# Performance work log

Measured on AMD Instinct MI355X. Metric: run time of the kernel, lower is better.

Reference implementation:

```python
import jax, jax.numpy as jnp
import numpy as np

N, E, G = 50000, 800000, 100
H, C = 4, 64


def _gatv2(x, src, dst, ea, Wl, bl, Wr, br, We, att, bias):
    # PyG GATv2Conv: x_l = lin_l(x) (source side), x_r = lin_r(x) (target side)
    xl = (x @ Wl + bl).reshape(-1, H, C)
    xr = (x @ Wr + br).reshape(-1, H, C)
    e = (ea @ We).reshape(-1, H, C)               # [E,H,C]
    m = jax.nn.leaky_relu(xl[src] + xr[dst] + e, negative_slope=0.2)
    alpha = jnp.einsum('ehc,hc->eh', m, att)      # [E,H]
    amax = jax.ops.segment_max(alpha, dst, num_segments=N)
    amax = jnp.where(jnp.isfinite(amax), amax, jnp.float32(0.0))
    ex = jnp.exp(alpha - amax[dst])
    denom = jax.ops.segment_sum(ex, dst, num_segments=N)
    a = ex / (denom[dst] + jnp.float32(1e-16))    # segment softmax over in-edges
    out = jax.ops.segment_sum(xl[src] * a[..., None], dst, num_segments=N)
    return out.reshape(N, H * C) + bias


def setup_inputs() -> dict:
    key = jax.random.key(0)
    ks = jax.random.split(key, 24)
    lin = lambda k, i, o: (jax.random.normal(k, (i, o), jnp.float32) / np.sqrt(i).astype(np.float32))
    x = jax.random.normal(ks[0], (N, 8), jnp.float32)
    edge_index = jnp.stack([jax.random.randint(ks[1], (E,), 0, N),
                            jax.random.randint(ks[2], (E,), 0, N)])
    edge_attr = jax.random.normal(ks[3], (E, 1), jnp.float32)
    batch = jnp.sort(jax.random.randint(ks[4], (N,), 0, G))
    return dict(
        x=x, edge_index=edge_index, edge_attr=edge_attr, batch=batch,
        enc_W=lin(ks[5], 8, 64), enc_b=jnp.zeros((64,), jnp.float32),
        g1_Wl=lin(ks[6], 64, 256), g1_bl=jnp.zeros((256,), jnp.float32),
        g1_Wr=lin(ks[7], 64, 256), g1_br=jnp.zeros((256,), jnp.float32),
        g1_We=lin(ks[8], 1, 256),
        g1_att=jax.random.normal(ks[9], (H, C), jnp.float32) / np.sqrt(C).astype(np.float32),
        g1_bias=jnp.zeros((256,), jnp.float32),
        g2_Wl=lin(ks[10], 256, 256), g2_bl=jnp.zeros((256,), jnp.float32),
        g2_Wr=lin(ks[11], 256, 256), g2_br=jnp.zeros((256,), jnp.float32),
        g2_We=lin(ks[12], 1, 256),
        g2_att=jax.random.normal(ks[13], (H, C), jnp.float32) / np.sqrt(C).astype(np.float32),
        g2_bias=jnp.zeros((256,), jnp.float32),
        p1_W=lin(ks[14], 256, 128), p1_b=jnp.zeros((128,), jnp.float32),
        ln_g=jnp.ones((128,), jnp.float32), ln_b=jnp.zeros((128,), jnp.float32),
        p2_W=lin(ks[15], 128, 64), p2_b=jnp.zeros((64,), jnp.float32),
    )


def reference(x, edge_index, edge_attr, batch,
              enc_W, enc_b,
              g1_Wl, g1_bl, g1_Wr, g1_br, g1_We, g1_att, g1_bias,
              g2_Wl, g2_bl, g2_Wr, g2_br, g2_We, g2_att, g2_bias,
              p1_W, p1_b, ln_g, ln_b, p2_W, p2_b):
    src, dst = edge_index[0], edge_index[1]
    h = jax.nn.relu(x @ enc_W + enc_b)
    h = jax.nn.relu(_gatv2(h, src, dst, edge_attr, g1_Wl, g1_bl, g1_Wr, g1_br, g1_We, g1_att, g1_bias))
    h = jax.nn.relu(_gatv2(h, src, dst, edge_attr, g2_Wl, g2_bl, g2_Wr, g2_br, g2_We, g2_att, g2_bias))
    # global mean pool over graphs
    sums = jax.ops.segment_sum(h, batch, num_segments=G)
    cnt = jax.ops.segment_sum(jnp.ones((N, 1), h.dtype), batch, num_segments=G)
    p = sums / jnp.maximum(cnt, jnp.float32(1.0))
    # post MLP (dropout is identity in eval)
    z = p @ p1_W + p1_b
    mu = jnp.mean(z, axis=-1, keepdims=True)
    var = jnp.mean(jnp.square(z - mu), axis=-1, keepdims=True)
    z = (z - mu) * jax.lax.rsqrt(var + jnp.float32(1e-5)) * ln_g + ln_b
    z = jax.nn.relu(z)
    return jax.nn.relu(z @ p2_W + p2_b)
```

## Files before the change

### kernel.cpp

```cpp
#include <hip/hip_runtime.h>

#define NH 4
#define CH 64

__global__ void encoder_kernel(const float* __restrict__ x, const float* __restrict__ W,
                               const float* __restrict__ b, float* __restrict__ h, int N) {
  int idx = blockIdx.x * blockDim.x + threadIdx.x;
  if (idx >= N * 64) return;
  int n = idx >> 6, j = idx & 63;
  const float* xp = x + n * 8;
  float acc = b[j];
#pragma unroll
  for (int k = 0; k < 8; ++k) acc = fmaf(xp[k], W[k * 64 + j], acc);
  h[idx] = fmaxf(acc, 0.0f);
}

template <int K>
__global__ void lin_lr_kernel(const float* __restrict__ h,
                              const float* __restrict__ Wl, const float* __restrict__ bl,
                              const float* __restrict__ Wr, const float* __restrict__ br,
                              float* __restrict__ xl, float* __restrict__ xr, int N) {
  __shared__ float hs[8][K];
  int n0 = blockIdx.x * 8;
  int j = threadIdx.x;
  int nmax = N - n0; if (nmax > 8) nmax = 8;
  for (int idx = j; idx < nmax * K; idx += 256) {
    int m = idx / K, k = idx % K;
    hs[m][k] = h[(size_t)(n0 + m) * K + k];
  }
  __syncthreads();
  float accl[8], accr[8];
  float bjl = bl[j], bjr = br[j];
#pragma unroll
  for (int m = 0; m < 8; ++m) { accl[m] = bjl; accr[m] = bjr; }
  for (int k = 0; k < K; ++k) {
    float wl = Wl[k * 256 + j];
    float wr = Wr[k * 256 + j];
#pragma unroll
    for (int m = 0; m < 8; ++m) {
      accl[m] = fmaf(hs[m][k], wl, accl[m]);
      accr[m] = fmaf(hs[m][k], wr, accr[m]);
    }
  }
  for (int m = 0; m < nmax; ++m) {
    xl[(size_t)(n0 + m) * 256 + j] = accl[m];
    xr[(size_t)(n0 + m) * 256 + j] = accr[m];
  }
}

__global__ void hist_kernel(const int* __restrict__ dst, int* __restrict__ deg, int E) {
  int e = blockIdx.x * blockDim.x + threadIdx.x;
  if (e < E) atomicAdd(&deg[dst[e]], 1);
}

__global__ void scan_partial_kernel(const int* __restrict__ deg, int* __restrict__ partial, int N) {
  __shared__ int sm[256];
  int t = threadIdx.x;
  int i = blockIdx.x * 256 + t;
  sm[t] = (i < N) ? deg[i] : 0;
  __syncthreads();
#pragma unroll
  for (int s = 128; s > 0; s >>= 1) {
    if (t < s) sm[t] += sm[t + s];
    __syncthreads();
  }
  if (t == 0) partial[blockIdx.x] = sm[0];
}

__global__ void scan_offsets_kernel(int* __restrict__ partial, int nb) {
  __shared__ int sm[256];
  int t = threadIdx.x;
  int v = (t < nb) ? partial[t] : 0;
  sm[t] = v;
  __syncthreads();
#pragma unroll
  for (int off = 1; off < 256; off <<= 1) {
    int a = (t >= off) ? sm[t - off] : 0;
    __syncthreads();
    sm[t] += a;
    __syncthreads();
  }
  if (t < nb) partial[t] = sm[t] - v;
}

__global__ void scan_final_kernel(const int* __restrict__ deg, const int* __restrict__ partial,
                                  int* __restrict__ rowptr, int* __restrict__ cursor, int N, int E) {
  __shared__ int sm[256];
  int t = threadIdx.x;
  int i = blockIdx.x * 256 + t;
  int v = (i < N) ? deg[i] : 0;
  sm[t] = v;
  __syncthreads();
#pragma unroll
  for (int off = 1; off < 256; off <<= 1) {
    int a = (t >= off) ? sm[t - off] : 0;
    __syncthreads();
    sm[t] += a;
    __syncthreads();
  }
  if (i < N) {
    int ex = partial[blockIdx.x] + sm[t] - v;
    rowptr[i] = ex;
    cursor[i] = ex;
  }
  if (i == 0) rowptr[N] = E;
}

__global__ void scatter_build_kernel(const int* __restrict__ src, const int* __restrict__ dst,
                                     const float* __restrict__ ea, int* __restrict__ cursor,
                                     int* __restrict__ srcs, float* __restrict__ eas, int E) {
  int e = blockIdx.x * blockDim.x + threadIdx.x;
  if (e >= E) return;
  int d = dst[e];
  int pos = atomicAdd(&cursor[d], 1);
  srcs[pos] = src[e];
  eas[pos] = ea[e];
}

__device__ __forceinline__ void edge_accum(const float4 xlv, const float eav,
                                           const float4 xr4, const float4 We4, const float4 at4,
                                           float4& acc, float& denom) {
  float4 v;
  v.x = fmaf(eav, We4.x, xlv.x + xr4.x);
  v.y = fmaf(eav, We4.y, xlv.y + xr4.y);
  v.z = fmaf(eav, We4.z, xlv.z + xr4.z);
  v.w = fmaf(eav, We4.w, xlv.w + xr4.w);
  v.x = (v.x >= 0.f) ? v.x : 0.2f * v.x;
  v.y = (v.y >= 0.f) ? v.y : 0.2f * v.y;
  v.z = (v.z >= 0.f) ? v.z : 0.2f * v.z;
  v.w = (v.w >= 0.f) ? v.w : 0.2f * v.w;
  float p = v.x * at4.x + v.y * at4.y + v.z * at4.z + v.w * at4.w;
  p += __shfl_xor(p, 1, 64);
  p += __shfl_xor(p, 2, 64);
  p += __shfl_xor(p, 4, 64);
  p += __shfl_xor(p, 8, 64);
  float ex = __expf(p);
  denom += ex;
  acc.x = fmaf(ex, xlv.x, acc.x);
  acc.y = fmaf(ex, xlv.y, acc.y);
  acc.z = fmaf(ex, xlv.z, acc.z);
  acc.w = fmaf(ex, xlv.w, acc.w);
}

template <bool POOL>
__global__ void gat_aggregate_kernel(const int* __restrict__ rowptr,
                                     const int* __restrict__ srcs,
                                     const float* __restrict__ eas,
                                     const float* __restrict__ xl,
                                     const float* __restrict__ xr,
                                     const float* __restrict__ We,
                                     const float* __restrict__ att,
                                     const float* __restrict__ bias,
                                     float* __restrict__ out,
                                     const int* __restrict__ batch,
                                     float* __restrict__ sums,
                                     float* __restrict__ cnt,
                                     int N) {
  int d = (int)((blockIdx.x * (size_t)blockDim.x + threadIdx.x) >> 6);
  int lane = threadIdx.x & 63;
  if (d >= N) return;
  const float4* xl4p = (const float4*)xl;
  float4 xr4 = ((const float4*)xr)[(size_t)d * 64 + lane];
  float4 We4 = ((const float4*)We)[lane];
  float4 at4 = ((const float4*)att)[lane];
  int beg = rowptr[d], end = rowptr[d + 1];
  float4 acc = {0.f, 0.f, 0.f, 0.f};
  float denom = 0.f;
  int i = beg;
  for (; i + 3 < end; i += 4) {
    int s0 = srcs[i], s1 = srcs[i + 1], s2 = srcs[i + 2], s3 = srcs[i + 3];
    float e0 = eas[i], e1 = eas[i + 1], e2 = eas[i + 2], e3 = eas[i + 3];
    float4 a0 = xl4p[(size_t)s0 * 64 + lane];
    float4 a1 = xl4p[(size_t)s1 * 64 + lane];
    float4 a2 = xl4p[(size_t)s2 * 64 + lane];
    float4 a3 = xl4p[(size_t)s3 * 64 + lane];
    edge_accum(a0, e0, xr4, We4, at4, acc, denom);
    edge_accum(a1, e1, xr4, We4, at4, acc, denom);
    edge_accum(a2, e2, xr4, We4, at4, acc, denom);
    edge_accum(a3, e3, xr4, We4, at4, acc, denom);
  }
  for (; i < end; ++i) {
    int s0 = srcs[i];
    float e0 = eas[i];
    float4 a0 = xl4p[(size_t)s0 * 64 + lane];
    edge_accum(a0, e0, xr4, We4, at4, acc, denom);
  }
  float inv = 1.f / (denom + 1e-16f);
  float4 b4 = ((const float4*)bias)[lane];
  float4 o;
  o.x = fmaxf(fmaf(acc.x, inv, b4.x), 0.f);
  o.y = fmaxf(fmaf(acc.y, inv, b4.y), 0.f);
  o.z = fmaxf(fmaf(acc.z, inv, b4.z), 0.f);
  o.w = fmaxf(fmaf(acc.w, inv, b4.w), 0.f);
  if (POOL) {
    int g = batch[d];
    float* sg = sums + (size_t)g * 256 + lane * 4;
    atomicAdd(sg + 0, o.x);
    atomicAdd(sg + 1, o.y);
    atomicAdd(sg + 2, o.z);
    atomicAdd(sg + 3, o.w);
    if (lane == 0) atomicAdd(&cnt[g], 1.0f);
  } else {
    ((float4*)out)[(size_t)d * 64 + lane] = o;
  }
}

__global__ void mlp_kernel(const float* __restrict__ sums, const float* __restrict__ cnt,
                           const float* __restrict__ p1W, const float* __restrict__ p1b,
                           const float* __restrict__ lng, const float* __restrict__ lnb,
                           const float* __restrict__ p2W, const float* __restrict__ p2b,
                           float* __restrict__ outp, int G) {
  __shared__ float p[256];
  __shared__ float z[128];
  __shared__ float wsum[2];
  __shared__ float wsum2[2];
  int g = blockIdx.x;
  int t = threadIdx.x;
  float c = fmaxf(cnt[g], 1.0f);
  p[t] = sums[(size_t)g * 256 + t] / c;
  p[t + 128] = sums[(size_t)g * 256 + t + 128] / c;
  __syncthreads();
  float acc = p1b[t];
  for (int k = 0; k < 256; ++k) acc = fmaf(p[k], p1W[k * 128 + t], acc);
  float v = acc;
#pragma unroll
  for (int off = 32; off > 0; off >>= 1) v += __shfl_xor(v, off, 64);
  if ((t & 63) == 0) wsum[t >> 6] = v;
  __syncthreads();
  float mu = (wsum[0] + wsum[1]) * (1.0f / 128.0f);
  float dv = acc - mu;
  float vv = dv * dv;
#pragma unroll
  for (int off = 32; off > 0; off >>= 1) vv += __shfl_xor(vv, off, 64);
  if ((t & 63) == 0) wsum2[t >> 6] = vv;
  __syncthreads();
  float var = (wsum2[0] + wsum2[1]) * (1.0f / 128.0f);
  float zv = dv * rsqrtf(var + 1e-5f) * lng[t] + lnb[t];
  z[t] = fmaxf(zv, 0.0f);
  __syncthreads();
  if (t < 64) {
    float o = p2b[t];
    for (int k = 0; k < 128; ++k) o = fmaf(z[k], p2W[k * 64 + t], o);
    outp[(size_t)g * 64 + t] = fmaxf(o, 0.0f);
  }
}

extern "C" void kernel_launch(void* const* d_in, const int* in_sizes, int n_in,
                              void* d_out, int out_size, void* d_ws, size_t ws_size,
                              hipStream_t stream) {
  const float* x      = (const float*)d_in[0];
  const int*   ei     = (const int*)d_in[1];
  const float* ea     = (const float*)d_in[2];
  const int*   batch  = (const int*)d_in[3];
  const float* enc_W  = (const float*)d_in[4];
  const float* enc_b  = (const float*)d_in[5];
  const float* Wl1    = (const float*)d_in[6];
  const float* bl1    = (const float*)d_in[7];
  const float* Wr1    = (const float*)d_in[8];
  const float* br1    = (const float*)d_in[9];
  const float* We1    = (const float*)d_in[10];
  const float* att1   = (const float*)d_in[11];
  const float* bias1  = (const float*)d_in[12];
  const float* Wl2    = (const float*)d_in[13];
  const float* bl2    = (const float*)d_in[14];
  const float* Wr2    = (const float*)d_in[15];
  const float* br2    = (const float*)d_in[16];
  const float* We2    = (const float*)d_in[17];
  const float* att2   = (const float*)d_in[18];
  const float* bias2  = (const float*)d_in[19];
  const float* p1W    = (const float*)d_in[20];
  const float* p1b    = (const float*)d_in[21];
  const float* lng    = (const float*)d_in[22];
  const float* lnb    = (const float*)d_in[23];
  const float* p2W    = (const float*)d_in[24];
  const float* p2b    = (const float*)d_in[25];
  float* outp = (float*)d_out;

  int N = in_sizes[0] / 8;
  int E = in_sizes[2];
  int G = out_size / 64;
  const int* src = ei;
  const int* dst = ei + E;
  int nb = (N + 255) / 256;

  float* ws      = (float*)d_ws;
  float* h0      = ws;
  float* B0      = h0     + (size_t)N * 64;
  float* B1      = B0     + (size_t)N * 256;
  float* B2      = B1     + (size_t)N * 256;
  float* eas     = B2     + (size_t)N * 256;
  float* sums    = eas    + (size_t)E;
  float* cnt     = sums   + (size_t)G * 256;
  int*   srcs    = (int*)(cnt + G);
  int*   rowptr  = srcs + (size_t)E;
  int*   cursor  = rowptr + (size_t)(N + 1);
  int*   partial = cursor + (size_t)N;

  encoder_kernel<<<(N * 64 + 255) / 256, 256, 0, stream>>>(x, enc_W, enc_b, h0, N);

  hipMemsetAsync(cursor, 0, (size_t)N * sizeof(int), stream);
  hist_kernel<<<(E + 255) / 256, 256, 0, stream>>>(dst, cursor, E);
  scan_partial_kernel<<<nb, 256, 0, stream>>>(cursor, partial, N);
  scan_offsets_kernel<<<1, 256, 0, stream>>>(partial, nb);
  scan_final_kernel<<<nb, 256, 0, stream>>>(cursor, partial, rowptr, cursor, N, E);
  scatter_build_kernel<<<(E + 255) / 256, 256, 0, stream>>>(src, dst, ea, cursor, srcs, eas, E);

  lin_lr_kernel<64><<<(N + 7) / 8, 256, 0, stream>>>(h0, Wl1, bl1, Wr1, br1, B0, B1, N);
  gat_aggregate_kernel<false><<<(N + 3) / 4, 256, 0, stream>>>(
      rowptr, srcs, eas, B0, B1, We1, att1, bias1, B2, nullptr, nullptr, nullptr, N);

  lin_lr_kernel<256><<<(N + 7) / 8, 256, 0, stream>>>(B2, Wl2, bl2, Wr2, br2, B0, B1, N);
  hipMemsetAsync(sums, 0, ((size_t)G * 256 + G) * sizeof(float), stream);
  gat_aggregate_kernel<true><<<(N + 3) / 4, 256, 0, stream>>>(
      rowptr, srcs, eas, B0, B1, We2, att2, bias2, nullptr, batch, sums, cnt, N);

  mlp_kernel<<<G, 128, 0, stream>>>(sums, cnt, p1W, p1b, lng, lnb, p2W, p2b, outp, G);
}
```

Before: 1.036 ms.

## Store source features in bf16 and pack edge src/attr into int2

The source-side projection xl is written as bf16 and widened back to float inside the aggregation, which halves the bytes of the random gather that dominates the edge loop. Edge source index and attribute are packed into a single int2 array so each edge costs one load instead of two. The main loop is unrolled to 8 edges, with a 2-edge and a 1-edge tail, to keep more gathers in flight. The cost is bf16 rounding error on xl, which feeds both the attention logits and the aggregated messages.

```diff
diff --git a/kernel.cpp b/kernel.cpp
--- a/kernel.cpp
+++ b/kernel.cpp
@@ -2,6 +2,14 @@
 
 #define NH 4
 #define CH 64
+
+__device__ __forceinline__ float bf2f(unsigned short u) {
+  return __uint_as_float(((unsigned)u) << 16);
+}
+__device__ __forceinline__ unsigned short f2bf(float f) {
+  unsigned b = __float_as_uint(f);
+  return (unsigned short)((b + 0x7fffu + ((b >> 16) & 1u)) >> 16);
+}
 
 __global__ void encoder_kernel(const float* __restrict__ x, const float* __restrict__ W,
                                const float* __restrict__ b, float* __restrict__ h, int N) {
@@ -19,7 +27,7 @@
 __global__ void lin_lr_kernel(const float* __restrict__ h,
                               const float* __restrict__ Wl, const float* __restrict__ bl,
                               const float* __restrict__ Wr, const float* __restrict__ br,
-                              float* __restrict__ xl, float* __restrict__ xr, int N) {
+                              unsigned short* __restrict__ xlb, float* __restrict__ xr, int N) {
   __shared__ float hs[8][K];
   int n0 = blockIdx.x * 8;
   int j = threadIdx.x;
@@ -43,7 +51,7 @@
     }
   }
   for (int m = 0; m < nmax; ++m) {
-    xl[(size_t)(n0 + m) * 256 + j] = accl[m];
+    xlb[(size_t)(n0 + m) * 256 + j] = f2bf(accl[m]);
     xr[(size_t)(n0 + m) * 256 + j] = accr[m];
   }
 }
@@ -108,18 +116,19 @@
 
 __global__ void scatter_build_kernel(const int* __restrict__ src, const int* __restrict__ dst,
                                      const float* __restrict__ ea, int* __restrict__ cursor,
-                                     int* __restrict__ srcs, float* __restrict__ eas, int E) {
+                                     int2* __restrict__ edg, int E) {
   int e = blockIdx.x * blockDim.x + threadIdx.x;
   if (e >= E) return;
   int d = dst[e];
   int pos = atomicAdd(&cursor[d], 1);
-  srcs[pos] = src[e];
-  eas[pos] = ea[e];
-}
-
-__device__ __forceinline__ void edge_accum(const float4 xlv, const float eav,
+  edg[pos] = make_int2(src[e], __float_as_int(ea[e]));
+}
+
+__device__ __forceinline__ void edge_accum(const ushort4 xu, const float eav,
                                            const float4 xr4, const float4 We4, const float4 at4,
                                            float4& acc, float& denom) {
+  float4 xlv;
+  xlv.x = bf2f(xu.x); xlv.y = bf2f(xu.y); xlv.z = bf2f(xu.z); xlv.w = bf2f(xu.w);
   float4 v;
   v.x = fmaf(eav, We4.x, xlv.x + xr4.x);
   v.y = fmaf(eav, We4.y, xlv.y + xr4.y);
@@ -144,9 +153,8 @@
 
 template <bool POOL>
 __global__ void gat_aggregate_kernel(const int* __restrict__ rowptr,
-                                     const int* __restrict__ srcs,
-                                     const float* __restrict__ eas,
-                                     const float* __restrict__ xl,
+                                     const int2* __restrict__ edg,
+                                     const unsigned short* __restrict__ xlb,
                                      const float* __restrict__ xr,
                                      const float* __restrict__ We,
                                      const float* __restrict__ att,
@@ -159,7 +167,7 @@
   int d = (int)((blockIdx.x * (size_t)blockDim.x + threadIdx.x) >> 6);
   int lane = threadIdx.x & 63;
   if (d >= N) return;
-  const float4* xl4p = (const float4*)xl;
+  const ushort4* xlp = (const ushort4*)xlb;
   float4 xr4 = ((const float4*)xr)[(size_t)d * 64 + lane];
   float4 We4 = ((const float4*)We)[lane];
   float4 at4 = ((const float4*)att)[lane];
@@ -167,23 +175,37 @@
   float4 acc = {0.f, 0.f, 0.f, 0.f};
   float denom = 0.f;
   int i = beg;
-  for (; i + 3 < end; i += 4) {
-    int s0 = srcs[i], s1 = srcs[i + 1], s2 = srcs[i + 2], s3 = srcs[i + 3];
-    float e0 = eas[i], e1 = eas[i + 1], e2 = eas[i + 2], e3 = eas[i + 3];
-    float4 a0 = xl4p[(size_t)s0 * 64 + lane];
-    float4 a1 = xl4p[(size_t)s1 * 64 + lane];
-    float4 a2 = xl4p[(size_t)s2 * 64 + lane];
-    float4 a3 = xl4p[(size_t)s3 * 64 + lane];
-    edge_accum(a0, e0, xr4, We4, at4, acc, denom);
-    edge_accum(a1, e1, xr4, We4, at4, acc, denom);
-    edge_accum(a2, e2, xr4, We4, at4, acc, denom);
-    edge_accum(a3, e3, xr4, We4, at4, acc, denom);
-  }
-  for (; i < end; ++i) {
-    int s0 = srcs[i];
-    float e0 = eas[i];
-    float4 a0 = xl4p[(size_t)s0 * 64 + lane];
-    edge_accum(a0, e0, xr4, We4, at4, acc, denom);
+  for (; i + 7 < end; i += 8) {
+    int2 e0 = edg[i], e1 = edg[i + 1], e2 = edg[i + 2], e3 = edg[i + 3];
+    int2 e4 = edg[i + 4], e5 = edg[i + 5], e6 = edg[i + 6], e7 = edg[i + 7];
+    ushort4 a0 = xlp[(size_t)e0.x * 64 + lane];
+    ushort4 a1 = xlp[(size_t)e1.x * 64 + lane];
+    ushort4 a2 = xlp[(size_t)e2.x * 64 + lane];
+    ushort4 a3 = xlp[(size_t)e3.x * 64 + lane];
+    ushort4 a4 = xlp[(size_t)e4.x * 64 + lane];
+    ushort4 a5 = xlp[(size_t)e5.x * 64 + lane];
+    ushort4 a6 = xlp[(size_t)e6.x * 64 + lane];
+    ushort4 a7 = xlp[(size_t)e7.x * 64 + lane];
+    edge_accum(a0, __int_as_float(e0.y), xr4, We4, at4, acc, denom);
+    edge_accum(a1, __int_as_float(e1.y), xr4, We4, at4, acc, denom);
+    edge_accum(a2, __int_as_float(e2.y), xr4, We4, at4, acc, denom);
+    edge_accum(a3, __int_as_float(e3.y), xr4, We4, at4, acc, denom);
+    edge_accum(a4, __int_as_float(e4.y), xr4, We4, at4, acc, denom);
+    edge_accum(a5, __int_as_float(e5.y), xr4, We4, at4, acc, denom);
+    edge_accum(a6, __int_as_float(e6.y), xr4, We4, at4, acc, denom);
+    edge_accum(a7, __int_as_float(e7.y), xr4, We4, at4, acc, denom);
+  }
+  for (; i + 1 < end; i += 2) {
+    int2 e0 = edg[i], e1 = edg[i + 1];
+    ushort4 a0 = xlp[(size_t)e0.x * 64 + lane];
+    ushort4 a1 = xlp[(size_t)e1.x * 64 + lane];
+    edge_accum(a0, __int_as_float(e0.y), xr4, We4, at4, acc, denom);
+    edge_accum(a1, __int_as_float(e1.y), xr4, We4, at4, acc, denom);
+  }
+  if (i < end) {
+    int2 e0 = edg[i];
+    ushort4 a0 = xlp[(size_t)e0.x * 64 + lane];
+    edge_accum(a0, __int_as_float(e0.y), xr4, We4, at4, acc, denom);
   }
   float inv = 1.f / (denom + 1e-16f);
   float4 b4 = ((const float4*)bias)[lane];
@@ -285,14 +307,13 @@
 
   float* ws      = (float*)d_ws;
   float* h0      = ws;
-  float* B0      = h0     + (size_t)N * 64;
-  float* B1      = B0     + (size_t)N * 256;
+  float* B1      = h0     + (size_t)N * 64;
   float* B2      = B1     + (size_t)N * 256;
-  float* eas     = B2     + (size_t)N * 256;
-  float* sums    = eas    + (size_t)E;
+  float* sums    = B2     + (size_t)N * 256;
   float* cnt     = sums   + (size_t)G * 256;
-  int*   srcs    = (int*)(cnt + G);
-  int*   rowptr  = srcs + (size_t)E;
+  unsigned short* xlb = (unsigned short*)(cnt + G);
+  int2*  edg     = (int2*)(xlb + (size_t)N * 256);
+  int*   rowptr  = (int*)(edg + (size_t)E);
   int*   cursor  = rowptr + (size_t)(N + 1);
   int*   partial = cursor + (size_t)N;
 
@@ -303,16 +324,16 @@
   scan_partial_kernel<<<nb, 256, 0, stream>>>(cursor, partial, N);
   scan_offsets_kernel<<<1, 256, 0, stream>>>(partial, nb);
   scan_final_kernel<<<nb, 256, 0, stream>>>(cursor, partial, rowptr, cursor, N, E);
-  scatter_build_kernel<<<(E + 255) / 256, 256, 0, stream>>>(src, dst, ea, cursor, srcs, eas, E);
-
-  lin_lr_kernel<64><<<(N + 7) / 8, 256, 0, stream>>>(h0, Wl1, bl1, Wr1, br1, B0, B1, N);
+  scatter_build_kernel<<<(E + 255) / 256, 256, 0, stream>>>(src, dst, ea, cursor, edg, E);
+
+  lin_lr_kernel<64><<<(N + 7) / 8, 256, 0, stream>>>(h0, Wl1, bl1, Wr1, br1, xlb, B1, N);
   gat_aggregate_kernel<false><<<(N + 3) / 4, 256, 0, stream>>>(
-      rowptr, srcs, eas, B0, B1, We1, att1, bias1, B2, nullptr, nullptr, nullptr, N);
-
-  lin_lr_kernel<256><<<(N + 7) / 8, 256, 0, stream>>>(B2, Wl2, bl2, Wr2, br2, B0, B1, N);
+      rowptr, edg, xlb, B1, We1, att1, bias1, B2, nullptr, nullptr, nullptr, N);
+
+  lin_lr_kernel<256><<<(N + 7) / 8, 256, 0, stream>>>(B2, Wl2, bl2, Wr2, br2, xlb, B1, N);
   hipMemsetAsync(sums, 0, ((size_t)G * 256 + G) * sizeof(float), stream);
   gat_aggregate_kernel<true><<<(N + 3) / 4, 256, 0, stream>>>(
-      rowptr, srcs, eas, B0, B1, We2, att2, bias2, nullptr, batch, sums, cnt, N);
+      rowptr, edg, xlb, B1, We2, att2, bias2, nullptr, batch, sums, cnt, N);
 
   mlp_kernel<<<G, 128, 0, stream>>>(sums, cnt, p1W, p1b, lng, lnb, p2W, p2b, outp, G);
 }
```

After: 1.053 ms. About the same (+1.7%).

## Pack edge src/attr into int2, load per-wave edge chunks, software-pipeline gathers

Applied to the files above, without the earlier changes.

The src index and edge attribute arrays are interleaved into a single int2 CSR array. Each wavefront loads up to 64 edges at once with one coalesced read and hands indices out by shuffle, replacing per-lane redundant scalar loads. The inner loop is software-pipelined so the next four xl row gathers are issued before the current four are accumulated. The trade-off is more register pressure and extra shuffles, and the workspace is padded because the chunk load can read past the end of the edge array.

```diff
diff --git a/kernel.cpp b/kernel.cpp
--- a/kernel.cpp
+++ b/kernel.cpp
@@ -108,13 +108,12 @@
 
 __global__ void scatter_build_kernel(const int* __restrict__ src, const int* __restrict__ dst,
                                      const float* __restrict__ ea, int* __restrict__ cursor,
-                                     int* __restrict__ srcs, float* __restrict__ eas, int E) {
+                                     int2* __restrict__ edg, int E) {
   int e = blockIdx.x * blockDim.x + threadIdx.x;
   if (e >= E) return;
   int d = dst[e];
   int pos = atomicAdd(&cursor[d], 1);
-  srcs[pos] = src[e];
-  eas[pos] = ea[e];
+  edg[pos] = make_int2(src[e], __float_as_int(ea[e]));
 }
 
 __device__ __forceinline__ void edge_accum(const float4 xlv, const float eav,
@@ -143,48 +142,70 @@
 }
 
 template <bool POOL>
-__global__ void gat_aggregate_kernel(const int* __restrict__ rowptr,
-                                     const int* __restrict__ srcs,
-                                     const float* __restrict__ eas,
-                                     const float* __restrict__ xl,
-                                     const float* __restrict__ xr,
-                                     const float* __restrict__ We,
-                                     const float* __restrict__ att,
-                                     const float* __restrict__ bias,
-                                     float* __restrict__ out,
-                                     const int* __restrict__ batch,
-                                     float* __restrict__ sums,
-                                     float* __restrict__ cnt,
-                                     int N) {
+__global__ __launch_bounds__(256) void gat_aggregate_kernel(
+    const int* __restrict__ rowptr, const int2* __restrict__ edg,
+    const float* __restrict__ xl, const float* __restrict__ xr,
+    const float* __restrict__ We, const float* __restrict__ att,
+    const float* __restrict__ bias, float* __restrict__ out,
+    const int* __restrict__ batch, float* __restrict__ sums, float* __restrict__ cnt,
+    int N) {
   int d = (int)((blockIdx.x * (size_t)blockDim.x + threadIdx.x) >> 6);
   int lane = threadIdx.x & 63;
   if (d >= N) return;
-  const float4* xl4p = (const float4*)xl;
+  const float4* xlp = (const float4*)xl;
   float4 xr4 = ((const float4*)xr)[(size_t)d * 64 + lane];
   float4 We4 = ((const float4*)We)[lane];
   float4 at4 = ((const float4*)att)[lane];
   int beg = rowptr[d], end = rowptr[d + 1];
   float4 acc = {0.f, 0.f, 0.f, 0.f};
   float denom = 0.f;
-  int i = beg;
-  for (; i + 3 < end; i += 4) {
-    int s0 = srcs[i], s1 = srcs[i + 1], s2 = srcs[i + 2], s3 = srcs[i + 3];
-    float e0 = eas[i], e1 = eas[i + 1], e2 = eas[i + 2], e3 = eas[i + 3];
-    float4 a0 = xl4p[(size_t)s0 * 64 + lane];
-    float4 a1 = xl4p[(size_t)s1 * 64 + lane];
-    float4 a2 = xl4p[(size_t)s2 * 64 + lane];
-    float4 a3 = xl4p[(size_t)s3 * 64 + lane];
-    edge_accum(a0, e0, xr4, We4, at4, acc, denom);
-    edge_accum(a1, e1, xr4, We4, at4, acc, denom);
-    edge_accum(a2, e2, xr4, We4, at4, acc, denom);
-    edge_accum(a3, e3, xr4, We4, at4, acc, denom);
-  }
-  for (; i < end; ++i) {
-    int s0 = srcs[i];
-    float e0 = eas[i];
-    float4 a0 = xl4p[(size_t)s0 * 64 + lane];
-    edge_accum(a0, e0, xr4, We4, at4, acc, denom);
-  }
+
+  for (int cb = beg; cb < end; cb += 64) {
+    int L = end - cb; if (L > 64) L = 64;
+    int2 m = edg[cb + lane];
+    float mea = __int_as_float(m.y);
+    int j = 0;
+    float4 c0, c1, c2, c3;
+    float ce0, ce1, ce2, ce3;
+    if (j + 3 < L) {
+      int s0 = __shfl(m.x, 0), s1 = __shfl(m.x, 1), s2 = __shfl(m.x, 2), s3 = __shfl(m.x, 3);
+      ce0 = __shfl(mea, 0); ce1 = __shfl(mea, 1); ce2 = __shfl(mea, 2); ce3 = __shfl(mea, 3);
+      c0 = xlp[(size_t)s0 * 64 + lane];
+      c1 = xlp[(size_t)s1 * 64 + lane];
+      c2 = xlp[(size_t)s2 * 64 + lane];
+      c3 = xlp[(size_t)s3 * 64 + lane];
+    }
+    for (; j + 7 < L; j += 4) {
+      int s0 = __shfl(m.x, j + 4), s1 = __shfl(m.x, j + 5);
+      int s2 = __shfl(m.x, j + 6), s3 = __shfl(m.x, j + 7);
+      float ne0 = __shfl(mea, j + 4), ne1 = __shfl(mea, j + 5);
+      float ne2 = __shfl(mea, j + 6), ne3 = __shfl(mea, j + 7);
+      float4 n0 = xlp[(size_t)s0 * 64 + lane];
+      float4 n1 = xlp[(size_t)s1 * 64 + lane];
+      float4 n2 = xlp[(size_t)s2 * 64 + lane];
+      float4 n3 = xlp[(size_t)s3 * 64 + lane];
+      edge_accum(c0, ce0, xr4, We4, at4, acc, denom);
+      edge_accum(c1, ce1, xr4, We4, at4, acc, denom);
+      edge_accum(c2, ce2, xr4, We4, at4, acc, denom);
+      edge_accum(c3, ce3, xr4, We4, at4, acc, denom);
+      c0 = n0; c1 = n1; c2 = n2; c3 = n3;
+      ce0 = ne0; ce1 = ne1; ce2 = ne2; ce3 = ne3;
+    }
+    if (j + 3 < L) {
+      edge_accum(c0, ce0, xr4, We4, at4, acc, denom);
+      edge_accum(c1, ce1, xr4, We4, at4, acc, denom);
+      edge_accum(c2, ce2, xr4, We4, at4, acc, denom);
+      edge_accum(c3, ce3, xr4, We4, at4, acc, denom);
+      j += 4;
+    }
+    for (; j < L; ++j) {
+      int s0 = __shfl(m.x, j);
+      float e0 = __shfl(mea, j);
+      float4 a0 = xlp[(size_t)s0 * 64 + lane];
+      edge_accum(a0, e0, xr4, We4, at4, acc, denom);
+    }
+  }
+
   float inv = 1.f / (denom + 1e-16f);
   float4 b4 = ((const float4*)bias)[lane];
   float4 o;
@@ -288,11 +309,10 @@
   float* B0      = h0     + (size_t)N * 64;
   float* B1      = B0     + (size_t)N * 256;
   float* B2      = B1     + (size_t)N * 256;
-  float* eas     = B2     + (size_t)N * 256;
-  float* sums    = eas    + (size_t)E;
+  float* sums    = B2     + (size_t)N * 256;
   float* cnt     = sums   + (size_t)G * 256;
-  int*   srcs    = (int*)(cnt + G);
-  int*   rowptr  = srcs + (size_t)E;
+  int2*  edg     = (int2*)(cnt + G);
+  int*   rowptr  = (int*)(edg + (size_t)E + 64);
   int*   cursor  = rowptr + (size_t)(N + 1);
   int*   partial = cursor + (size_t)N;
 
@@ -303,16 +323,16 @@
   scan_partial_kernel<<<nb, 256, 0, stream>>>(cursor, partial, N);
   scan_offsets_kernel<<<1, 256, 0, stream>>>(partial, nb);
   scan_final_kernel<<<nb, 256, 0, stream>>>(cursor, partial, rowptr, cursor, N, E);
-  scatter_build_kernel<<<(E + 255) / 256, 256, 0, stream>>>(src, dst, ea, cursor, srcs, eas, E);
+  scatter_build_kernel<<<(E + 255) / 256, 256, 0, stream>>>(src, dst, ea, cursor, edg, E);
 
   lin_lr_kernel<64><<<(N + 7) / 8, 256, 0, stream>>>(h0, Wl1, bl1, Wr1, br1, B0, B1, N);
   gat_aggregate_kernel<false><<<(N + 3) / 4, 256, 0, stream>>>(
-      rowptr, srcs, eas, B0, B1, We1, att1, bias1, B2, nullptr, nullptr, nullptr, N);
+      rowptr, edg, B0, B1, We1, att1, bias1, B2, nullptr, nullptr, nullptr, N);
 
   lin_lr_kernel<256><<<(N + 7) / 8, 256, 0, stream>>>(B2, Wl2, bl2, Wr2, br2, B0, B1, N);
   hipMemsetAsync(sums, 0, ((size_t)G * 256 + G) * sizeof(float), stream);
   gat_aggregate_kernel<true><<<(N + 3) / 4, 256, 0, stream>>>(
-      rowptr, srcs, eas, B0, B1, We2, att2, bias2, nullptr, batch, sums, cnt, N);
+      rowptr, edg, B0, B1, We2, att2, bias2, nullptr, batch, sums, cnt, N);
 
   mlp_kernel<<<G, 128, 0, stream>>>(sums, cnt, p1W, p1b, lng, lnb, p2W, p2b, outp, G);
 }
```

Result: slower. 1.081 ms (+4.4%).
